# Optimization experiments

Measured on AMD Instinct MI355X. Metric: run time of the kernel, lower is better.

The kernel has to match this reference:

```python
import jax, jax.numpy as jnp
import numpy as np

N = 200000
F_IN = 128
F_OUT = 128
NBRS = 4  # NEIGHBORHOOD_SIZE - 1 (self counted separately)


def setup_inputs() -> dict:
    key = jax.random.key(0)
    k1, k2, k3, k4, k5 = jax.random.split(key, 5)
    features = jax.random.normal(k1, (N, F_IN), dtype=jnp.float32)
    prev_features = jax.random.normal(k2, (N, F_IN), dtype=jnp.float32)
    neighbor_idx = jax.random.randint(k3, (N, NBRS), 0, N, dtype=jnp.int32)
    # nn.Linear(5*in, out): weight [out, 5*in], bias [out]
    W = jax.random.normal(k4, (F_OUT, 5 * F_IN), dtype=jnp.float32) * 0.02
    b = jax.random.normal(k5, (F_OUT,), dtype=jnp.float32) * 0.02
    return {"features": features, "prev_features": prev_features,
            "neighbor_idx": neighbor_idx, "W": W, "b": b}


def reference(features, prev_features, neighbor_idx, W, b):
    # gather neighbor prev_features: [N, 4, F_IN] -> [N, 4*F_IN]
    nbr = prev_features[neighbor_idx].reshape(N, NBRS * F_IN)
    # concat self features first (matches torch loop order): [N, 5*F_IN]
    gathered = jnp.concatenate([features, nbr], axis=1)
    # linear: y = gathered @ W^T + b -> [N, F_OUT]
    new_features = jnp.einsum('nk,ok->no', gathered, W) + b
    # module sets tet.features = new_features and prev_features = features;
    # both end up equal to new_features.
    return new_features
```

## Files before the change

### kernel.cpp

```cpp
#include <hip/hip_runtime.h>


#define N_PTS  200000
#define F_INN  128
#define K_TOT  640
#define NCT    4

typedef __attribute__((ext_vector_type(8)))  short bf16x8;
typedef __attribute__((ext_vector_type(16))) float f32x16;
typedef __attribute__((ext_vector_type(8)))  float f32x8;

union Frag { bf16x8 v; unsigned int u[4]; };

__device__ __forceinline__ unsigned int bf_rne_bits(float f) {
    unsigned int u = __builtin_bit_cast(unsigned int, f);
    return (u + 0x7FFFu + ((u >> 16) & 1u)) & 0xFFFF0000u;
}

__device__ __forceinline__ void split8_rne(const f32x8 a, bf16x8& hi, bf16x8& lo) {
    Frag H, L;
#pragma unroll
    for (int p = 0; p < 4; ++p) {
        float f0 = a[2 * p], f1 = a[2 * p + 1];
        unsigned int h0 = bf_rne_bits(f0), h1 = bf_rne_bits(f1);
        float r0 = f0 - __builtin_bit_cast(float, h0);
        float r1 = f1 - __builtin_bit_cast(float, h1);
        unsigned int l0 = bf_rne_bits(r0), l1 = bf_rne_bits(r1);
        H.u[p] = (h0 >> 16) | h1;
        L.u[p] = (l0 >> 16) | l1;
    }
    hi = H.v; lo = L.v;
}

__device__ __forceinline__ void split8_trunc(const f32x8 a, bf16x8& hi, bf16x8& lo) {
    Frag H, L;
#pragma unroll
    for (int p = 0; p < 4; ++p) {
        float f0 = a[2 * p], f1 = a[2 * p + 1];
        unsigned int u0 = __builtin_bit_cast(unsigned int, f0);
        unsigned int u1 = __builtin_bit_cast(unsigned int, f1);
        unsigned int h0 = u0 & 0xFFFF0000u, h1 = u1 & 0xFFFF0000u;
        float r0 = f0 - __builtin_bit_cast(float, h0);
        float r1 = f1 - __builtin_bit_cast(float, h1);
        unsigned int l0 = __builtin_bit_cast(unsigned int, r0);
        unsigned int l1 = __builtin_bit_cast(unsigned int, r1);
        H.u[p] = (h0 >> 16) | h1;
        L.u[p] = (l0 >> 16) | (l1 & 0xFFFF0000u);
    }
    hi = H.v; lo = L.v;
}

__global__ void build_wf(const float* __restrict__ W, bf16x8* __restrict__ wfbuf) {
    int tid = blockIdx.x * blockDim.x + threadIdx.x;
    int lane = tid & 63;
    int ct   = (tid >> 6) & 3;
    int t    = tid >> 8;
    if (t >= 40) return;
    int c = ct * 32 + (lane & 31);
    int k = t * 16 + (lane >> 5) * 8;
    f32x8 w = *(const f32x8*)(W + (size_t)c * K_TOT + k);
    bf16x8 h, l;
    split8_rne(w, h, l);
    wfbuf[((t * 4 + ct) * 2 + 0) * 64 + lane] = h;
    wfbuf[((t * 4 + ct) * 2 + 1) * 64 + lane] = l;
}

__global__ __launch_bounds__(256, 2)
void mcconv(const float* __restrict__ feat, const float* __restrict__ prev,
            const int* __restrict__ nbr, const float* __restrict__ bias,
            const char* __restrict__ wfbuf, float* __restrict__ out) {
    __shared__ char smem[2 * 32768];

    const int lane = threadIdx.x & 63;
    const int wave = threadIdx.x >> 6;
    const int g    = lane >> 5;
    const int r31  = lane & 31;
    const int n0   = blockIdx.x * 256 + wave * 64;

    int nA  = n0 + r31;
    int nB  = n0 + 32 + r31;
    int nAc = nA < N_PTS ? nA : N_PTS - 1;
    int nBc = nB < N_PTS ? nB : N_PTS - 1;
    const int4 iA = *(const int4*)(nbr + 4 * (size_t)nAc);
    const int4 iB = *(const int4*)(nbr + 4 * (size_t)nBc);

    const float* s0A = feat + (size_t)nAc  * F_INN;
    const float* s0B = feat + (size_t)nBc  * F_INN;
    const float* s1A = prev + (size_t)iA.x * F_INN;
    const float* s1B = prev + (size_t)iB.x * F_INN;
    const float* s2A = prev + (size_t)iA.y * F_INN;
    const float* s2B = prev + (size_t)iB.y * F_INN;
    const float* s3A = prev + (size_t)iA.z * F_INN;
    const float* s3B = prev + (size_t)iB.z * F_INN;
    const float* s4A = prev + (size_t)iA.w * F_INN;
    const float* s4B = prev + (size_t)iB.w * F_INN;

    f32x16 acc[2][NCT];
#pragma unroll
    for (int m = 0; m < 2; ++m)
#pragma unroll
        for (int c = 0; c < NCT; ++c)
#pragma unroll
            for (int i = 0; i < 16; ++i) acc[m][c][i] = 0.0f;

    auto STAGE = [&](int buf, int phase) {
        const char* gsrc = wfbuf + (size_t)phase * 32768 + wave * 8192 + lane * 16;
        char* ldst = smem + buf * 32768 + wave * 8192;
#pragma unroll
        for (int i = 0; i < 8; ++i) {
            __builtin_amdgcn_global_load_lds(
                (const __attribute__((address_space(1))) unsigned int*)(gsrc + i * 1024),
                (__attribute__((address_space(3))) unsigned int*)(ldst + i * 1024),
                16, 0, 0);
        }
    };

    STAGE(0, 0);
    __syncthreads();

    for (int p = 0; p < 10; ++p) {
        const int cur = p & 1;
        if (p < 9) STAGE(cur ^ 1, p + 1);

        const int s   = p >> 1;
        const int cc0 = (p & 1) * 4;
        const float *pA, *pB;
        if      (s == 0) { pA = s0A; pB = s0B; }
        else if (s == 1) { pA = s1A; pB = s1B; }
        else if (s == 2) { pA = s2A; pB = s2B; }
        else if (s == 3) { pA = s3A; pB = s3B; }
        else             { pA = s4A; pB = s4B; }

        const char* fb = smem + cur * 32768;
#pragma unroll
        for (int c = 0; c < 4; ++c) {
            const int cc = cc0 + c;
            f32x8 aA = *(const f32x8*)(pA + cc * 16 + g * 8);
            f32x8 aB = *(const f32x8*)(pB + cc * 16 + g * 8);
            bf16x8 ahA, alA, ahB, alB;
            split8_trunc(aA, ahA, alA);
            split8_trunc(aB, ahB, alB);
#pragma unroll
            for (int ct = 0; ct < NCT; ++ct) {
                bf16x8 bh = *(const bf16x8*)(fb + c * 8192 + ct * 2048 +        lane * 16);
                bf16x8 bl = *(const bf16x8*)(fb + c * 8192 + ct * 2048 + 1024 + lane * 16);
                acc[0][ct] = __builtin_amdgcn_mfma_f32_32x32x16_bf16(ahA, bh, acc[0][ct], 0, 0, 0);
                acc[0][ct] = __builtin_amdgcn_mfma_f32_32x32x16_bf16(alA, bh, acc[0][ct], 0, 0, 0);
                acc[0][ct] = __builtin_amdgcn_mfma_f32_32x32x16_bf16(ahA, bl, acc[0][ct], 0, 0, 0);
                acc[1][ct] = __builtin_amdgcn_mfma_f32_32x32x16_bf16(ahB, bh, acc[1][ct], 0, 0, 0);
                acc[1][ct] = __builtin_amdgcn_mfma_f32_32x32x16_bf16(alB, bh, acc[1][ct], 0, 0, 0);
                acc[1][ct] = __builtin_amdgcn_mfma_f32_32x32x16_bf16(ahB, bl, acc[1][ct], 0, 0, 0);
            }
        }
        __syncthreads();
    }

    float bcol[NCT];
#pragma unroll
    for (int ct = 0; ct < NCT; ++ct) bcol[ct] = bias[ct * 32 + r31];

#pragma unroll
    for (int m = 0; m < 2; ++m) {
        const int nbase = n0 + m * 32 + 4 * g;
#pragma unroll
        for (int reg = 0; reg < 16; ++reg) {
            const int row = nbase + (reg & 3) + 8 * (reg >> 2);
            if (row < N_PTS) {
#pragma unroll
                for (int ct = 0; ct < NCT; ++ct)
                    out[(size_t)row * F_INN + ct * 32 + r31] = acc[m][ct][reg] + bcol[ct];
            }
        }
    }
}

extern "C" void kernel_launch(void* const* d_in, const int* in_sizes, int n_in,
                              void* d_out, int out_size, void* d_ws, size_t ws_size,
                              hipStream_t stream) {
    const float* feat = (const float*)d_in[0];
    const float* prev = (const float*)d_in[1];
    const int*   nbr  = (const int*)d_in[2];
    const float* W    = (const float*)d_in[3];
    const float* bias = (const float*)d_in[4];
    float* out = (float*)d_out;

    bf16x8* wfbuf = (bf16x8*)d_ws;

    hipLaunchKernelGGL(build_wf, dim3(40), dim3(256), 0, stream, W, wfbuf);

    const int grid = (N_PTS + 255) / 256;
    hipLaunchKernelGGL(mcconv, dim3(grid), dim3(256), 0, stream,
                       feat, prev, nbr, bias, (const char*)wfbuf, out);
}
```

Before: 338.3 us.

## Use 8 waves of 32 rows each and prefetch activations one phase ahead

Blocks grow from 4 to 8 waves, each wave now owning one 32-row M tile instead of two, which halves per-wave accumulator registers so more waves can be resident. The phase loop is unrolled into a ping-pong where the next phase's gathered feature rows are loaded into registers before the current phase is computed, so gather latency overlaps MFMA work. Weight staging into LDS is split across 8 waves. The cost is that each LDS weight fragment now feeds one M tile per wave instead of two, doubling LDS reads per MFMA, and the prefetch buffers add register pressure.

```diff
diff --git a/kernel.cpp b/kernel.cpp
--- a/kernel.cpp
+++ b/kernel.cpp
@@ -65,7 +65,7 @@
     wfbuf[((t * 4 + ct) * 2 + 1) * 64 + lane] = l;
 }
 
-__global__ __launch_bounds__(256, 2)
+__global__ __launch_bounds__(512, 2)
 void mcconv(const float* __restrict__ feat, const float* __restrict__ prev,
             const int* __restrict__ nbr, const float* __restrict__ bias,
             const char* __restrict__ wfbuf, float* __restrict__ out) {
@@ -75,39 +75,29 @@
     const int wave = threadIdx.x >> 6;
     const int g    = lane >> 5;
     const int r31  = lane & 31;
-    const int n0   = blockIdx.x * 256 + wave * 64;
+    const int n0   = blockIdx.x * 256 + wave * 32;
 
     int nA  = n0 + r31;
-    int nB  = n0 + 32 + r31;
     int nAc = nA < N_PTS ? nA : N_PTS - 1;
-    int nBc = nB < N_PTS ? nB : N_PTS - 1;
     const int4 iA = *(const int4*)(nbr + 4 * (size_t)nAc);
-    const int4 iB = *(const int4*)(nbr + 4 * (size_t)nBc);
 
-    const float* s0A = feat + (size_t)nAc  * F_INN;
-    const float* s0B = feat + (size_t)nBc  * F_INN;
-    const float* s1A = prev + (size_t)iA.x * F_INN;
-    const float* s1B = prev + (size_t)iB.x * F_INN;
-    const float* s2A = prev + (size_t)iA.y * F_INN;
-    const float* s2B = prev + (size_t)iB.y * F_INN;
-    const float* s3A = prev + (size_t)iA.z * F_INN;
-    const float* s3B = prev + (size_t)iB.z * F_INN;
-    const float* s4A = prev + (size_t)iA.w * F_INN;
-    const float* s4B = prev + (size_t)iB.w * F_INN;
+    const float* s0 = feat + (size_t)nAc  * F_INN;
+    const float* s1 = prev + (size_t)iA.x * F_INN;
+    const float* s2 = prev + (size_t)iA.y * F_INN;
+    const float* s3 = prev + (size_t)iA.z * F_INN;
+    const float* s4 = prev + (size_t)iA.w * F_INN;
 
-    f32x16 acc[2][NCT];
+    f32x16 acc[NCT];
 #pragma unroll
-    for (int m = 0; m < 2; ++m)
+    for (int c = 0; c < NCT; ++c)
 #pragma unroll
-        for (int c = 0; c < NCT; ++c)
-#pragma unroll
-            for (int i = 0; i < 16; ++i) acc[m][c][i] = 0.0f;
+        for (int i = 0; i < 16; ++i) acc[c][i] = 0.0f;
 
     auto STAGE = [&](int buf, int phase) {
-        const char* gsrc = wfbuf + (size_t)phase * 32768 + wave * 8192 + lane * 16;
-        char* ldst = smem + buf * 32768 + wave * 8192;
+        const char* gsrc = wfbuf + (size_t)phase * 32768 + wave * 4096 + lane * 16;
+        char* ldst = smem + buf * 32768 + wave * 4096;
 #pragma unroll
-        for (int i = 0; i < 8; ++i) {
+        for (int i = 0; i < 4; ++i) {
             __builtin_amdgcn_global_load_lds(
                 (const __attribute__((address_space(1))) unsigned int*)(gsrc + i * 1024),
                 (__attribute__((address_space(3))) unsigned int*)(ldst + i * 1024),
@@ -115,43 +105,50 @@
         }
     };
 
-    STAGE(0, 0);
-    __syncthreads();
+    auto PRE = [&](f32x8 (&dst)[4], int phase) {
+        const int s = phase >> 1;
+        const float* p = (s == 0) ? s0 : (s == 1) ? s1 : (s == 2) ? s2 : (s == 3) ? s3 : s4;
+        const int cc0 = (phase & 1) * 4;
+#pragma unroll
+        for (int c = 0; c < 4; ++c)
+            dst[c] = *(const f32x8*)(p + (cc0 + c) * 16 + g * 8);
+    };
 
-    for (int p = 0; p < 10; ++p) {
-        const int cur = p & 1;
-        if (p < 9) STAGE(cur ^ 1, p + 1);
-
-        const int s   = p >> 1;
-        const int cc0 = (p & 1) * 4;
-        const float *pA, *pB;
-        if      (s == 0) { pA = s0A; pB = s0B; }
-        else if (s == 1) { pA = s1A; pB = s1B; }
-        else if (s == 2) { pA = s2A; pB = s2B; }
-        else if (s == 3) { pA = s3A; pB = s3B; }
-        else             { pA = s4A; pB = s4B; }
-
-        const char* fb = smem + cur * 32768;
+    auto COMPUTE = [&](int buf, f32x8 (&a)[4]) {
+        const char* fb = smem + buf * 32768;
 #pragma unroll
         for (int c = 0; c < 4; ++c) {
-            const int cc = cc0 + c;
-            f32x8 aA = *(const f32x8*)(pA + cc * 16 + g * 8);
-            f32x8 aB = *(const f32x8*)(pB + cc * 16 + g * 8);
-            bf16x8 ahA, alA, ahB, alB;
-            split8_trunc(aA, ahA, alA);
-            split8_trunc(aB, ahB, alB);
+            bf16x8 ah, al;
+            split8_trunc(a[c], ah, al);
 #pragma unroll
             for (int ct = 0; ct < NCT; ++ct) {
                 bf16x8 bh = *(const bf16x8*)(fb + c * 8192 + ct * 2048 +        lane * 16);
                 bf16x8 bl = *(const bf16x8*)(fb + c * 8192 + ct * 2048 + 1024 + lane * 16);
-                acc[0][ct] = __builtin_amdgcn_mfma_f32_32x32x16_bf16(ahA, bh, acc[0][ct], 0, 0, 0);
-                acc[0][ct] = __builtin_amdgcn_mfma_f32_32x32x16_bf16(alA, bh, acc[0][ct], 0, 0, 0);
-                acc[0][ct] = __builtin_amdgcn_mfma_f32_32x32x16_bf16(ahA, bl, acc[0][ct], 0, 0, 0);
-                acc[1][ct] = __builtin_amdgcn_mfma_f32_32x32x16_bf16(ahB, bh, acc[1][ct], 0, 0, 0);
-                acc[1][ct] = __builtin_amdgcn_mfma_f32_32x32x16_bf16(alB, bh, acc[1][ct], 0, 0, 0);
-                acc[1][ct] = __builtin_amdgcn_mfma_f32_32x32x16_bf16(ahB, bl, acc[1][ct], 0, 0, 0);
+                acc[ct] = __builtin_amdgcn_mfma_f32_32x32x16_bf16(ah, bh, acc[ct], 0, 0, 0);
+                acc[ct] = __builtin_amdgcn_mfma_f32_32x32x16_bf16(al, bh, acc[ct], 0, 0, 0);
+                acc[ct] = __builtin_amdgcn_mfma_f32_32x32x16_bf16(ah, bl, acc[ct], 0, 0, 0);
             }
         }
+    };
+
+    f32x8 aA[4], aB[4];
+
+    PRE(aA, 0);
+    STAGE(0, 0);
+    __syncthreads();
+
+#pragma unroll
+    for (int pp = 0; pp < 5; ++pp) {
+        const int p0 = 2 * pp, p1 = 2 * pp + 1;
+        STAGE(1, p0 + 1);
+        PRE(aB, p0 + 1);
+        COMPUTE(0, aA);
+        __syncthreads();
+        if (p1 < 9) {
+            STAGE(0, p1 + 1);
+            PRE(aA, p1 + 1);
+        }
+        COMPUTE(1, aB);
         __syncthreads();
     }
 
@@ -160,16 +157,12 @@
     for (int ct = 0; ct < NCT; ++ct) bcol[ct] = bias[ct * 32 + r31];
 
 #pragma unroll
-    for (int m = 0; m < 2; ++m) {
-        const int nbase = n0 + m * 32 + 4 * g;
+    for (int reg = 0; reg < 16; ++reg) {
+        const int row = n0 + (reg & 3) + 8 * (reg >> 2) + 4 * g;
+        if (row < N_PTS) {
 #pragma unroll
-        for (int reg = 0; reg < 16; ++reg) {
-            const int row = nbase + (reg & 3) + 8 * (reg >> 2);
-            if (row < N_PTS) {
-#pragma unroll
-                for (int ct = 0; ct < NCT; ++ct)
-                    out[(size_t)row * F_INN + ct * 32 + r31] = acc[m][ct][reg] + bcol[ct];
-            }
+            for (int ct = 0; ct < NCT; ++ct)
+                out[(size_t)row * F_INN + ct * 32 + r31] = acc[ct][reg] + bcol[ct];
         }
     }
 }
@@ -189,6 +182,6 @@
     hipLaunchKernelGGL(build_wf, dim3(40), dim3(256), 0, stream, W, wfbuf);
 
     const int grid = (N_PTS + 255) / 256;
-    hipLaunchKernelGGL(mcconv, dim3(grid), dim3(256), 0, stream,
+    hipLaunchKernelGGL(mcconv, dim3(grid), dim3(512), 0, stream,
                        feat, prev, nbr, bias, (const char*)wfbuf, out);
 }
```

Result: slower. 345.9 us (+2.2%).
